# Kernel tuning notes

Hardware: AMD Instinct MI355X
Metric: run time of the kernel (lower is better)

The kernel has to match this reference:

```python
import jax, jax.numpy as jnp
import numpy as np

EMB = 768
HEADS = 12
DK = EMB // HEADS


def setup_inputs() -> dict:
    key = jax.random.key(0)
    ks = jax.random.split(key, 11)
    B, S = 2, 2048
    lim = 1.0 / np.sqrt(EMB)
    def lin(k):
        kw, kb = jax.random.split(k)
        W = jax.random.uniform(kw, (EMB, EMB), jnp.float32, -lim, lim)
        b = jax.random.uniform(kb, (EMB,), jnp.float32, -lim, lim)
        return W, b
    Wq, bq = lin(ks[0])
    Wk, bk = lin(ks[1])
    Wv, bv = lin(ks[2])
    Wo, bo = lin(ks[3])
    return {
        "query": jax.random.normal(ks[4], (B, S, EMB), jnp.float32),
        "key": jax.random.normal(ks[5], (B, S, EMB), jnp.float32),
        "value": jax.random.normal(ks[6], (B, S, EMB), jnp.float32),
        "Wq": Wq, "bq": bq, "Wk": Wk, "bk": bk,
        "Wv": Wv, "bv": bv, "Wo": Wo, "bo": bo,
    }


def reference(query, key, value, Wq, bq, Wk, bk, Wv, bv, Wo, bo):
    B, S, _ = query.shape
    # nn.Linear: x @ W^T + b, then split heads -> [B, H, S, d_k]
    def proj(x, W, b):
        return (x @ W.T + b).reshape(B, -1, HEADS, DK).transpose(0, 2, 1, 3)
    q = proj(query, Wq, bq)
    k = proj(key, Wk, bk)
    v = proj(value, Wv, bv)
    scale = 1.0 / jnp.sqrt(jnp.float32(DK))
    scores = jnp.einsum('bhqd,bhkd->bhqk', q, k) * scale  # [B,H,S,S]
    attn = jax.nn.softmax(scores, axis=-1)
    av = jnp.einsum('bhqk,bhkd->bhqd', attn, v)
    concat = av.transpose(0, 2, 1, 3).reshape(B, -1, EMB)
    return concat @ Wo.T + bo
```

## Files before the change

### kernel.cpp

```cpp
#include <hip/hip_runtime.h>
#include <hip/hip_bf16.h>

#define EMB 768
#define HEADS 12
#define DKV 64
#define BATCH 2
#define SEQ 2048
#define NTOK (BATCH*SEQ)

typedef float f32x4 __attribute__((ext_vector_type(4)));
typedef unsigned short u16;
typedef u16 u16x8 __attribute__((ext_vector_type(8)));
typedef u16 u16x4 __attribute__((ext_vector_type(4)));
typedef __bf16 bf16x8 __attribute__((ext_vector_type(8)));

__device__ __forceinline__ u16 f2bf(float f) {
  return __builtin_bit_cast(u16, (__bf16)f);
}
__device__ __forceinline__ float fexp2(float x) {
#if __has_builtin(__builtin_amdgcn_exp2f)
  return __builtin_amdgcn_exp2f(x);
#else
  return exp2f(x);
#endif
}
__device__ __forceinline__ f32x4 mfma16(u16x8 a, u16x8 b, f32x4 c) {
  return __builtin_amdgcn_mfma_f32_16x16x32_bf16(
      __builtin_bit_cast(bf16x8, a), __builtin_bit_cast(bf16x8, b), c, 0, 0, 0);
}
__device__ __forceinline__ void gload16(const void* g, void* l) {
  __builtin_amdgcn_global_load_lds(
      (const __attribute__((address_space(1))) void*)g,
      (__attribute__((address_space(3))) void*)l, 16, 0, 0);
}

__global__ void cast_all_k(
    const float* __restrict__ x0, const float* __restrict__ x1, const float* __restrict__ x2,
    const float* __restrict__ w0, const float* __restrict__ w1,
    const float* __restrict__ w2, const float* __restrict__ w3,
    u16* __restrict__ X0, u16* __restrict__ X1, u16* __restrict__ X2,
    u16* __restrict__ W0, u16* __restrict__ W1, u16* __restrict__ W2, u16* __restrict__ W3,
    float wscale0)
{
  const int NX = NTOK*EMB/8;
  const int NW = EMB*EMB/8;
  const int total = 3*NX + 4*NW;
  int i = blockIdx.x*256 + threadIdx.x;
  for (; i < total; i += gridDim.x*256) {
    const float* s; u16* d; int off; float sc = 1.f;
    if (i < 3*NX) {
      int which = i / NX; off = i - which*NX;
      s = which==0 ? x0 : which==1 ? x1 : x2;
      d = which==0 ? X0 : which==1 ? X1 : X2;
    } else {
      int j = i - 3*NX; int which = j / NW; off = j - which*NW;
      s = which==0 ? w0 : which==1 ? w1 : which==2 ? w2 : w3;
      d = which==0 ? W0 : which==1 ? W1 : which==2 ? W2 : W3;
      if (which == 0) sc = wscale0;
    }
    float4 a = reinterpret_cast<const float4*>(s)[off*2];
    float4 b = reinterpret_cast<const float4*>(s)[off*2+1];
    u16x8 o;
    o[0]=f2bf(a.x*sc); o[1]=f2bf(a.y*sc); o[2]=f2bf(a.z*sc); o[3]=f2bf(a.w*sc);
    o[4]=f2bf(b.x*sc); o[5]=f2bf(b.y*sc); o[6]=f2bf(b.z*sc); o[7]=f2bf(b.w*sc);
    reinterpret_cast<u16x8*>(d)[off] = o;
  }
}

template<int MODE>
__device__ __forceinline__ void gemm_core(
    const u16* __restrict__ A, const u16* __restrict__ Bm,
    const float* __restrict__ bias, float bscale, void* __restrict__ outp,
    u16* __restrict__ At, u16* __restrict__ Bt, int m0, int n0)
{
  const int t = threadIdx.x;
  const int w = t >> 6, lane = t & 63, lg = lane >> 4, lr = lane & 15;
  const int wr = w >> 1, wc = w & 1;

  f32x4 acc[2][4] = {};

  const int lrow = lane >> 3;
  const int csl  = lane & 7;

  auto STAGE = [&](int kb) {
    #pragma unroll
    for (int i = 0; i < 2; ++i) {
      int ci = w*2 + i;
      int row = ci*8 + lrow;
      int sg = csl ^ (row & 7);
      gload16(A + (size_t)(m0+row)*EMB + kb + sg*8, &At[ci*512]);
    }
    #pragma unroll
    for (int i = 0; i < 4; ++i) {
      int ci = w*4 + i;
      int row = ci*8 + lrow;
      int sg = csl ^ (row & 7);
      gload16(Bm + (size_t)(n0+row)*EMB + kb + sg*8, &Bt[ci*512]);
    }
  };

  auto COMPUTE = [&]() {
    u16x8 af[2][2], bf[4][2];
    #pragma unroll
    for (int fm = 0; fm < 2; ++fm)
      #pragma unroll
      for (int kk = 0; kk < 2; ++kk) {
        int r = wr*32 + fm*16 + lr;
        int p = (lg + 4*kk) ^ (r & 7);
        af[fm][kk] = *reinterpret_cast<const u16x8*>(&At[r*64 + p*8]);
      }
    #pragma unroll
    for (int fn = 0; fn < 4; ++fn)
      #pragma unroll
      for (int kk = 0; kk < 2; ++kk) {
        int r = wc*64 + fn*16 + lr;
        int p = (lg + 4*kk) ^ (r & 7);
        bf[fn][kk] = *reinterpret_cast<const u16x8*>(&Bt[r*64 + p*8]);
      }
    __builtin_amdgcn_s_setprio(1);
    #pragma unroll
    for (int fm = 0; fm < 2; ++fm)
      #pragma unroll
      for (int fn = 0; fn < 4; ++fn)
        #pragma unroll
        for (int kk = 0; kk < 2; ++kk)
          acc[fm][fn] = mfma16(af[fm][kk], bf[fn][kk], acc[fm][fn]);
    __builtin_amdgcn_s_setprio(0);
  };

  const int NSTEP = EMB/64;
  #pragma unroll
  for (int ts = 0; ts < NSTEP; ++ts) {
    STAGE(ts*64);
    __syncthreads();
    COMPUTE();
    if (ts+1 < NSTEP) __syncthreads();
  }

  #pragma unroll
  for (int fm = 0; fm < 2; ++fm)
    #pragma unroll
    for (int fn = 0; fn < 4; ++fn) {
      const int mb = m0 + wr*32 + fm*16 + lg*4;
      const int e  = n0 + wc*64 + fn*16 + lr;
      if constexpr (MODE == 2) {
        int bb = mb >> 11, sb = mb & 2047, h = e >> 6, d = e & 63;
        u16x4 o4;
        #pragma unroll
        for (int j = 0; j < 4; ++j) o4[j] = f2bf(acc[fm][fn][j] + bias[e]*bscale);
        *reinterpret_cast<u16x4*>(
            reinterpret_cast<u16*>(outp) + (((size_t)(bb*HEADS+h))*DKV + d)*SEQ + sb) = o4;
      } else {
        #pragma unroll
        for (int j = 0; j < 4; ++j) {
          int m = mb + j;
          float val = acc[fm][fn][j] + bias[e]*bscale;
          if constexpr (MODE == 0) {
            int bb = m >> 11, s = m & 2047, h = e >> 6, d = e & 63;
            reinterpret_cast<u16*>(outp)[(((size_t)(bb*HEADS+h))*SEQ + s)*DKV + d] = f2bf(val);
          } else {
            reinterpret_cast<float*>(outp)[(size_t)m*EMB + e] = val;
          }
        }
      }
    }
}

__global__ __launch_bounds__(256) void qkv_k(
    const u16* __restrict__ Xq, const u16* __restrict__ Xk, const u16* __restrict__ Xv,
    const u16* __restrict__ Wq, const u16* __restrict__ Wk, const u16* __restrict__ Wv,
    const float* __restrict__ bq, const float* __restrict__ bk, const float* __restrict__ bv,
    u16* __restrict__ Qh, u16* __restrict__ Kh, u16* __restrict__ Vh, float csc)
{
  __shared__ __align__(16) u16 At[64*64];
  __shared__ __align__(16) u16 Bt[128*64];
  const int m0 = blockIdx.x*64, n0 = blockIdx.y*128;
  const int z = blockIdx.z;
  if (z == 0)
    gemm_core<0>(Xq, Wq, bq, csc, Qh, At, Bt, m0, n0);
  else if (z == 1)
    gemm_core<0>(Xk, Wk, bk, 1.f, Kh, At, Bt, m0, n0);
  else
    gemm_core<2>(Xv, Wv, bv, 1.f, Vh, At, Bt, m0, n0);
}

__global__ __launch_bounds__(256) void gemm_out_k(
    const u16* __restrict__ A, const u16* __restrict__ Bm,
    const float* __restrict__ bias, float* __restrict__ outp)
{
  __shared__ __align__(16) u16 At[64*64];
  __shared__ __align__(16) u16 Bt[128*64];
  gemm_core<1>(A, Bm, bias, 1.f, outp, At, Bt, blockIdx.x*64, blockIdx.y*128);
}

__global__ __launch_bounds__(256) void flash_attn_k(
    const u16* __restrict__ Q, const u16* __restrict__ K, const u16* __restrict__ VT,
    u16* __restrict__ av)
{
  __shared__ __align__(16) u16 Kt[2][64*64];
  __shared__ __align__(16) u16 Vt[2][64*64];
  __shared__ __align__(16) u16 Pt[4][16*64];

  const int t = threadIdx.x;
  const int w = t >> 6, lane = t & 63, lg = lane >> 4, lr = lane & 15;
  const int tr = t >> 3, tsl = t & 7;
  const int qb = blockIdx.x;
  const int bh = blockIdx.y;
  const u16* Qb = Q  + (size_t)bh*SEQ*DKV;
  const u16* Kb = K  + (size_t)bh*SEQ*DKV;
  const u16* Vb = VT + (size_t)bh*DKV*SEQ;

  const int qrow = qb*64 + w*16 + lr;
  u16x8 qf[2];
  qf[0] = *reinterpret_cast<const u16x8*>(Qb + (size_t)qrow*DKV + lg*8);
  qf[1] = *reinterpret_cast<const u16x8*>(Qb + (size_t)qrow*DKV + 32 + lg*8);

  f32x4 acc[4] = {};
  float mrun = -1e30f, lrun = 0.f;

  u16x8 ks[2], vs[2];
  auto LOADKV = [&](int kt0) {
    #pragma unroll
    for (int q = 0; q < 2; ++q) {
      int row = q*32 + tr;
      ks[q] = *reinterpret_cast<const u16x8*>(Kb + (size_t)(kt0+row)*DKV + tsl*8);
    }
    #pragma unroll
    for (int q = 0; q < 2; ++q) {
      int d = q*32 + tr;
      vs[q] = *reinterpret_cast<const u16x8*>(Vb + (size_t)d*SEQ + kt0 + tsl*8);
    }
  };

  const int NT = SEQ/64;
  LOADKV(0);
  {
    #pragma unroll
    for (int q = 0; q < 2; ++q) {
      int row = q*32 + tr;
      *reinterpret_cast<u16x8*>(&Kt[0][row*64 + ((tsl ^ (row & 7))*8)]) = ks[q];
    }
    #pragma unroll
    for (int q = 0; q < 2; ++q) {
      int d = q*32 + tr;
      *reinterpret_cast<u16x8*>(&Vt[0][d*64 + ((tsl ^ (d & 7))*8)]) = vs[q];
    }
  }
  __syncthreads();

  char* Pw = reinterpret_cast<char*>(&Pt[w][0]);

#define TILE(bi, kt)                                                          \
  do {                                                                        \
    if ((kt)+1 < NT) LOADKV(((kt)+1)*64);                                     \
    f32x4 s[4];                                                               \
    __builtin_amdgcn_s_setprio(1);                                            \
    _Pragma("unroll")                                                         \
    for (int fc = 0; fc < 4; ++fc) {                                          \
      f32x4 z = {};                                                           \
      _Pragma("unroll")                                                       \
      for (int kk = 0; kk < 2; ++kk) {                                        \
        int r = fc*16 + lr;                                                   \
        int slot = (lg + 4*kk) ^ (r & 7);                                     \
        u16x8 kf = *reinterpret_cast<const u16x8*>(&Kt[bi][r*64 + slot*8]);   \
        z = mfma16(kf, qf[kk], z);                                            \
      }                                                                       \
      s[fc] = z;                                                              \
    }                                                                         \
    __builtin_amdgcn_s_setprio(0);                                            \
    float a0 = fmaxf(fmaxf(s[0][0], s[0][1]), s[0][2]);                       \
    float a1 = fmaxf(fmaxf(s[0][3], s[1][0]), s[1][1]);                       \
    float a2 = fmaxf(fmaxf(s[1][2], s[1][3]), s[2][0]);                       \
    float a3 = fmaxf(fmaxf(s[2][1], s[2][2]), s[2][3]);                       \
    float a4 = fmaxf(fmaxf(s[3][0], s[3][1]), s[3][2]);                       \
    float pmax = fmaxf(fmaxf(fmaxf(a0, a1), a2),                              \
                       fmaxf(fmaxf(a3, a4), s[3][3]));                        \
    if (__any(pmax > mrun + 8.f)) {          \
      float pm = fmaxf(pmax, __shfl_xor(pmax, 16));                           \
      pm = fmaxf(pm, __shfl_xor(pm, 32));                                     \
      float mnew = fmaxf(mrun, pm);                                           \
      float corr = fexp2(mrun - mnew);                                        \
      mrun = mnew; lrun *= corr;                                              \
      _Pragma("unroll")                                                       \
      for (int fc = 0; fc < 4; ++fc)                                          \
        _Pragma("unroll")                                                     \
        for (int j = 0; j < 4; ++j)                                           \
          acc[fc][j] *= corr;                                                 \
    }                                                                         \
    float p[4][4], rs[4];                                                     \
    _Pragma("unroll")                                                         \
    for (int fc = 0; fc < 4; ++fc) {                                          \
      _Pragma("unroll")                                                       \
      for (int j = 0; j < 4; ++j) p[fc][j] = fexp2(s[fc][j] - mrun);          \
      rs[fc] = (p[fc][0] + p[fc][1]) + (p[fc][2] + p[fc][3]);                 \
    }                                                                         \
    lrun += (rs[0] + rs[1]) + (rs[2] + rs[3]);      \
    _Pragma("unroll")                                                         \
    for (int fc = 0; fc < 4; ++fc) {                                          \
      u16x4 q4;                                                               \
      _Pragma("unroll")                                                       \
      for (int j = 0; j < 4; ++j) q4[j] = f2bf(p[fc][j]);                     \
      *reinterpret_cast<u16x4*>(                                              \
          Pw + lr*128 + (((fc*4 + lg) ^ ((lr & 7) << 1))*8)) = q4;            \
    }                                                                         \
    asm volatile("s_waitcnt lgkmcnt(0)" ::: "memory");                        \
    __builtin_amdgcn_sched_barrier(0);                                        \
    __builtin_amdgcn_s_setprio(1);                                            \
    _Pragma("unroll")                                                         \
    for (int kk = 0; kk < 2; ++kk) {                                          \
      u16x8 pf = *reinterpret_cast<const u16x8*>(                             \
          Pw + lr*128 + (((kk*8 + lg*2) ^ ((lr & 7) << 1))*8));               \
      _Pragma("unroll")                                                       \
      for (int fc = 0; fc < 4; ++fc) {                                        \
        int rv = fc*16 + lr;                                                  \
        int slotv = (lg + 4*kk) ^ (rv & 7);                                   \
        u16x8 vf = *reinterpret_cast<const u16x8*>(&Vt[bi][rv*64 + slotv*8]); \
        acc[fc] = mfma16(vf, pf, acc[fc]);                                    \
      }                                                                       \
    }                                                                         \
    __builtin_amdgcn_s_setprio(0);                                            \
    if ((kt)+1 < NT) {                                                        \
      _Pragma("unroll")                                                       \
      for (int q = 0; q < 2; ++q) {                                           \
        int row = q*32 + tr;                                                  \
        *reinterpret_cast<u16x8*>(                                            \
            &Kt[(bi)^1][row*64 + ((tsl ^ (row & 7))*8)]) = ks[q];             \
      }                                                                       \
      _Pragma("unroll")                                                       \
      for (int q = 0; q < 2; ++q) {                                           \
        int d = q*32 + tr;                                                    \
        *reinterpret_cast<u16x8*>(                                            \
            &Vt[(bi)^1][d*64 + ((tsl ^ (d & 7))*8)]) = vs[q];                 \
      }                                                                       \
    }                                                                         \
    __syncthreads();                                                          \
  } while (0)

  for (int kt = 0; kt < NT; kt += 2) {
    TILE(0, kt);
    TILE(1, kt+1);
  }
#undef TILE

  float lt = lrun;
  lt += __shfl_xor(lt, 16);
  lt += __shfl_xor(lt, 32);
  const float inv = 1.0f / lt;

  const int b = bh / HEADS, h = bh % HEADS;
  #pragma unroll
  for (int fc = 0; fc < 4; ++fc) {
    u16x4 o4;
    #pragma unroll
    for (int j = 0; j < 4; ++j) o4[j] = f2bf(acc[fc][j] * inv);
    *reinterpret_cast<u16x4*>(
        av + ((size_t)(b*SEQ + qrow))*EMB + h*64 + fc*16 + lg*4) = o4;
  }
}

extern "C" void kernel_launch(void* const* d_in, const int* in_sizes, int n_in,
                              void* d_out, int out_size, void* d_ws, size_t ws_size,
                              hipStream_t stream) {
  const float* xq_f = (const float*)d_in[0];
  const float* xk_f = (const float*)d_in[1];
  const float* xv_f = (const float*)d_in[2];
  const float* Wq = (const float*)d_in[3];
  const float* bq = (const float*)d_in[4];
  const float* Wk = (const float*)d_in[5];
  const float* bk = (const float*)d_in[6];
  const float* Wv = (const float*)d_in[7];
  const float* bv = (const float*)d_in[8];
  const float* Wo = (const float*)d_in[9];
  const float* bo = (const float*)d_in[10];

  const size_t NX = (size_t)NTOK*EMB;
  const size_t NW = (size_t)EMB*EMB;
  u16* Xc0 = (u16*)d_ws;
  u16* Xc1 = Xc0 + NX;
  u16* Xc2 = Xc1 + NX;
  u16* Wc0 = Xc2 + NX;
  u16* Wc1 = Wc0 + NW;
  u16* Wc2 = Wc1 + NW;
  u16* Wc3 = Wc2 + NW;
  u16* Qh  = Wc3 + NW;
  u16* Kh  = Qh + NX;
  u16* Vh  = Kh + NX;
  u16* Xb  = Xc0;

  const float csc = 0.125f * 1.4426950408889634f;

  cast_all_k<<<dim3(2048), dim3(256), 0, stream>>>(
      xq_f, xk_f, xv_f, Wq, Wk, Wv, Wo,
      Xc0, Xc1, Xc2, Wc0, Wc1, Wc2, Wc3, csc);

  qkv_k<<<dim3(NTOK/64, EMB/128, 3), dim3(256), 0, stream>>>(
      Xc0, Xc1, Xc2, Wc0, Wc1, Wc2, bq, bk, bv, Qh, Kh, Vh, csc);

  flash_attn_k<<<dim3(SEQ/64, BATCH*HEADS), dim3(256), 0, stream>>>(Qh, Kh, Vh, Xb);

  gemm_out_k<<<dim3(NTOK/64, EMB/128), dim3(256), 0, stream>>>(Xb, Wc3, bo, (float*)d_out);
}
```

Before: 96.39 us.

## Fuse activation fp32-to-bf16 cast into QKV GEMM and use async LDS loads in attention

```diff
diff --git a/kernel.cpp b/kernel.cpp
--- a/kernel.cpp
+++ b/kernel.cpp
@@ -34,62 +34,72 @@
       (__attribute__((address_space(3))) void*)l, 16, 0, 0);
 }
 
-__global__ void cast_all_k(
-    const float* __restrict__ x0, const float* __restrict__ x1, const float* __restrict__ x2,
+__global__ void cast_w_k(
     const float* __restrict__ w0, const float* __restrict__ w1,
     const float* __restrict__ w2, const float* __restrict__ w3,
-    u16* __restrict__ X0, u16* __restrict__ X1, u16* __restrict__ X2,
-    u16* __restrict__ W0, u16* __restrict__ W1, u16* __restrict__ W2, u16* __restrict__ W3,
-    float wscale0)
+    u16* __restrict__ W0, u16* __restrict__ W1, u16* __restrict__ W2, u16* __restrict__ W3)
 {
-  const int NX = NTOK*EMB/8;
   const int NW = EMB*EMB/8;
-  const int total = 3*NX + 4*NW;
   int i = blockIdx.x*256 + threadIdx.x;
-  for (; i < total; i += gridDim.x*256) {
-    const float* s; u16* d; int off; float sc = 1.f;
-    if (i < 3*NX) {
-      int which = i / NX; off = i - which*NX;
-      s = which==0 ? x0 : which==1 ? x1 : x2;
-      d = which==0 ? X0 : which==1 ? X1 : X2;
-    } else {
-      int j = i - 3*NX; int which = j / NW; off = j - which*NW;
-      s = which==0 ? w0 : which==1 ? w1 : which==2 ? w2 : w3;
-      d = which==0 ? W0 : which==1 ? W1 : which==2 ? W2 : W3;
-      if (which == 0) sc = wscale0;
-    }
-    float4 a = reinterpret_cast<const float4*>(s)[off*2];
-    float4 b = reinterpret_cast<const float4*>(s)[off*2+1];
-    u16x8 o;
-    o[0]=f2bf(a.x*sc); o[1]=f2bf(a.y*sc); o[2]=f2bf(a.z*sc); o[3]=f2bf(a.w*sc);
-    o[4]=f2bf(b.x*sc); o[5]=f2bf(b.y*sc); o[6]=f2bf(b.z*sc); o[7]=f2bf(b.w*sc);
-    reinterpret_cast<u16x8*>(d)[off] = o;
-  }
-}
-
-template<int MODE>
+  if (i >= 4*NW) return;
+  int which = i / NW, off = i - which*NW;
+  const float* s = which==0 ? w0 : which==1 ? w1 : which==2 ? w2 : w3;
+  u16* d        = which==0 ? W0 : which==1 ? W1 : which==2 ? W2 : W3;
+  float4 a = reinterpret_cast<const float4*>(s)[off*2];
+  float4 b = reinterpret_cast<const float4*>(s)[off*2+1];
+  u16x8 o;
+  o[0]=f2bf(a.x); o[1]=f2bf(a.y); o[2]=f2bf(a.z); o[3]=f2bf(a.w);
+  o[4]=f2bf(b.x); o[5]=f2bf(b.y); o[6]=f2bf(b.z); o[7]=f2bf(b.w);
+  reinterpret_cast<u16x8*>(d)[off] = o;
+}
+
+template<int MODE, bool AF32>
 __device__ __forceinline__ void gemm_core(
-    const u16* __restrict__ A, const u16* __restrict__ Bm,
-    const float* __restrict__ bias, float bscale, void* __restrict__ outp,
-    u16* __restrict__ At, u16* __restrict__ Bt, int m0, int n0)
+    const void* __restrict__ Ap, const u16* __restrict__ Bm,
+    const float* __restrict__ bias, float ascale, float bscale,
+    void* __restrict__ outp, u16* __restrict__ At, u16* __restrict__ Bt,
+    int m0, int n0)
 {
   const int t = threadIdx.x;
   const int w = t >> 6, lane = t & 63, lg = lane >> 4, lr = lane & 15;
   const int wr = w >> 1, wc = w & 1;
+  const int lrow = lane >> 3, csl = lane & 7;
 
   f32x4 acc[2][4] = {};
-
-  const int lrow = lane >> 3;
-  const int csl  = lane & 7;
-
-  auto STAGE = [&](int kb) {
+  f32x4 raf[2][2];
+
+  auto A_LOAD = [&](int kb) {
+    #pragma unroll
+    for (int q2 = 0; q2 < 2; ++q2) {
+      int c = q2*256 + t, row = c >> 3, sl = c & 7;
+      const float* p = (const float*)Ap + (size_t)(m0+row)*EMB + kb + sl*8;
+      raf[q2][0] = *reinterpret_cast<const f32x4*>(p);
+      raf[q2][1] = *reinterpret_cast<const f32x4*>(p + 4);
+    }
+  };
+  auto A_WRITE = [&]() {
+    #pragma unroll
+    for (int q2 = 0; q2 < 2; ++q2) {
+      int c = q2*256 + t, row = c >> 3, sl = c & 7;
+      u16x8 v;
+      #pragma unroll
+      for (int j = 0; j < 4; ++j) {
+        v[j]   = f2bf(raf[q2][0][j] * ascale);
+        v[4+j] = f2bf(raf[q2][1][j] * ascale);
+      }
+      *reinterpret_cast<u16x8*>(&At[row*64 + ((sl ^ (row & 7))*8)]) = v;
+    }
+  };
+  auto A_GLOAD = [&](int kb) {
     #pragma unroll
     for (int i = 0; i < 2; ++i) {
       int ci = w*2 + i;
       int row = ci*8 + lrow;
       int sg = csl ^ (row & 7);
-      gload16(A + (size_t)(m0+row)*EMB + kb + sg*8, &At[ci*512]);
-    }
+      gload16((const u16*)Ap + (size_t)(m0+row)*EMB + kb + sg*8, &At[ci*512]);
+    }
+  };
+  auto B_GLOAD = [&](int kb) {
     #pragma unroll
     for (int i = 0; i < 4; ++i) {
       int ci = w*4 + i;
@@ -129,12 +139,31 @@
   };
 
   const int NSTEP = EMB/64;
-  #pragma unroll
-  for (int ts = 0; ts < NSTEP; ++ts) {
-    STAGE(ts*64);
+  if constexpr (AF32) {
+    A_LOAD(0);
+    B_GLOAD(0);
+    A_WRITE();
     __syncthreads();
-    COMPUTE();
-    if (ts+1 < NSTEP) __syncthreads();
+    #pragma unroll
+    for (int ts = 0; ts < NSTEP; ++ts) {
+      if (ts+1 < NSTEP) A_LOAD((ts+1)*64);
+      COMPUTE();
+      if (ts+1 < NSTEP) {
+        __syncthreads();
+        B_GLOAD((ts+1)*64);
+        A_WRITE();
+        __syncthreads();
+      }
+    }
+  } else {
+    #pragma unroll
+    for (int ts = 0; ts < NSTEP; ++ts) {
+      A_GLOAD(ts*64);
+      B_GLOAD(ts*64);
+      __syncthreads();
+      COMPUTE();
+      if (ts+1 < NSTEP) __syncthreads();
+    }
   }
 
   #pragma unroll
@@ -167,7 +196,7 @@
 }
 
 __global__ __launch_bounds__(256) void qkv_k(
-    const u16* __restrict__ Xq, const u16* __restrict__ Xk, const u16* __restrict__ Xv,
+    const float* __restrict__ Xq, const float* __restrict__ Xk, const float* __restrict__ Xv,
     const u16* __restrict__ Wq, const u16* __restrict__ Wk, const u16* __restrict__ Wv,
     const float* __restrict__ bq, const float* __restrict__ bk, const float* __restrict__ bv,
     u16* __restrict__ Qh, u16* __restrict__ Kh, u16* __restrict__ Vh, float csc)
@@ -177,11 +206,11 @@
   const int m0 = blockIdx.x*64, n0 = blockIdx.y*128;
   const int z = blockIdx.z;
   if (z == 0)
-    gemm_core<0>(Xq, Wq, bq, csc, Qh, At, Bt, m0, n0);
+    gemm_core<0,true>(Xq, Wq, bq, csc, csc, Qh, At, Bt, m0, n0);
   else if (z == 1)
-    gemm_core<0>(Xk, Wk, bk, 1.f, Kh, At, Bt, m0, n0);
+    gemm_core<0,true>(Xk, Wk, bk, 1.f, 1.f, Kh, At, Bt, m0, n0);
   else
-    gemm_core<2>(Xv, Wv, bv, 1.f, Vh, At, Bt, m0, n0);
+    gemm_core<2,true>(Xv, Wv, bv, 1.f, 1.f, Vh, At, Bt, m0, n0);
 }
 
 __global__ __launch_bounds__(256) void gemm_out_k(
@@ -190,7 +219,7 @@
 {
   __shared__ __align__(16) u16 At[64*64];
   __shared__ __align__(16) u16 Bt[128*64];
-  gemm_core<1>(A, Bm, bias, 1.f, outp, At, Bt, blockIdx.x*64, blockIdx.y*128);
+  gemm_core<1,false>(A, Bm, bias, 1.f, 1.f, outp, At, Bt, blockIdx.x*64, blockIdx.y*128);
 }
 
 __global__ __launch_bounds__(256) void flash_attn_k(
@@ -203,7 +232,6 @@
 
   const int t = threadIdx.x;
   const int w = t >> 6, lane = t & 63, lg = lane >> 4, lr = lane & 15;
-  const int tr = t >> 3, tsl = t & 7;
   const int qb = blockIdx.x;
   const int bh = blockIdx.y;
   const u16* Qb = Q  + (size_t)bh*SEQ*DKV;
@@ -218,41 +246,29 @@
   f32x4 acc[4] = {};
   float mrun = -1e30f, lrun = 0.f;
 
-  u16x8 ks[2], vs[2];
-  auto LOADKV = [&](int kt0) {
-    #pragma unroll
-    for (int q = 0; q < 2; ++q) {
-      int row = q*32 + tr;
-      ks[q] = *reinterpret_cast<const u16x8*>(Kb + (size_t)(kt0+row)*DKV + tsl*8);
-    }
-    #pragma unroll
-    for (int q = 0; q < 2; ++q) {
-      int d = q*32 + tr;
-      vs[q] = *reinterpret_cast<const u16x8*>(Vb + (size_t)d*SEQ + kt0 + tsl*8);
+  auto STAGE = [&](int kt0, int bi) {
+    #pragma unroll
+    for (int c2 = 0; c2 < 2; ++c2) {
+      int c = c2*256 + t;
+      int row = c >> 3, sl = c & 7;
+      int sg = sl ^ (row & 7);
+      gload16(Kb + (size_t)(kt0+row)*DKV + sg*8, &Kt[bi][c*8]);
+    }
+    #pragma unroll
+    for (int c2 = 0; c2 < 2; ++c2) {
+      int c = c2*256 + t;
+      int row = c >> 3, sl = c & 7;
+      int sg = sl ^ (row & 7);
+      gload16(Vb + (size_t)row*SEQ + kt0 + sg*8, &Vt[bi][c*8]);
     }
   };
 
   const int NT = SEQ/64;
-  LOADKV(0);
-  {
-    #pragma unroll
-    for (int q = 0; q < 2; ++q) {
-      int row = q*32 + tr;
-      *reinterpret_cast<u16x8*>(&Kt[0][row*64 + ((tsl ^ (row & 7))*8)]) = ks[q];
-    }
-    #pragma unroll
-    for (int q = 0; q < 2; ++q) {
-      int d = q*32 + tr;
-      *reinterpret_cast<u16x8*>(&Vt[0][d*64 + ((tsl ^ (d & 7))*8)]) = vs[q];
-    }
-  }
-  __syncthreads();
-
   char* Pw = reinterpret_cast<char*>(&Pt[w][0]);
 
 #define TILE(bi, kt)                                                          \
   do {                                                                        \
-    if ((kt)+1 < NT) LOADKV(((kt)+1)*64);                                     \
+    if ((kt)+1 < NT) STAGE(((kt)+1)*64, (bi)^1);    \
     f32x4 s[4];                                                               \
     __builtin_amdgcn_s_setprio(1);                                            \
     _Pragma("unroll")                                                         \
@@ -319,23 +335,11 @@
       }                                                                       \
     }                                                                         \
     __builtin_amdgcn_s_setprio(0);                                            \
-    if ((kt)+1 < NT) {                                                        \
-      _Pragma("unroll")                                                       \
-      for (int q = 0; q < 2; ++q) {                                           \
-        int row = q*32 + tr;                                                  \
-        *reinterpret_cast<u16x8*>(                                            \
-            &Kt[(bi)^1][row*64 + ((tsl ^ (row & 7))*8)]) = ks[q];             \
-      }                                                                       \
-      _Pragma("unroll")                                                       \
-      for (int q = 0; q < 2; ++q) {                                           \
-        int d = q*32 + tr;                                                    \
-        *reinterpret_cast<u16x8*>(                                            \
-            &Vt[(bi)^1][d*64 + ((tsl ^ (d & 7))*8)]) = vs[q];                 \
-      }                                                                       \
-    }                                                                         \
-    __syncthreads();                                                          \
+    __syncthreads();   \
   } while (0)
 
+  STAGE(0, 0);
+  __syncthreads();
   for (int kt = 0; kt < NT; kt += 2) {
     TILE(0, kt);
     TILE(1, kt+1);
@@ -375,26 +379,22 @@
 
   const size_t NX = (size_t)NTOK*EMB;
   const size_t NW = (size_t)EMB*EMB;
-  u16* Xc0 = (u16*)d_ws;
-  u16* Xc1 = Xc0 + NX;
-  u16* Xc2 = Xc1 + NX;
-  u16* Wc0 = Xc2 + NX;
+  u16* Wc0 = (u16*)d_ws;
   u16* Wc1 = Wc0 + NW;
   u16* Wc2 = Wc1 + NW;
   u16* Wc3 = Wc2 + NW;
   u16* Qh  = Wc3 + NW;
   u16* Kh  = Qh + NX;
   u16* Vh  = Kh + NX;
-  u16* Xb  = Xc0;
+  u16* Xb  = Vh + NX;
 
   const float csc = 0.125f * 1.4426950408889634f;
 
-  cast_all_k<<<dim3(2048), dim3(256), 0, stream>>>(
-      xq_f, xk_f, xv_f, Wq, Wk, Wv, Wo,
-      Xc0, Xc1, Xc2, Wc0, Wc1, Wc2, Wc3, csc);
+  cast_w_k<<<dim3(4*EMB*EMB/8/256), dim3(256), 0, stream>>>(
+      Wq, Wk, Wv, Wo, Wc0, Wc1, Wc2, Wc3);
 
   qkv_k<<<dim3(NTOK/64, EMB/128, 3), dim3(256), 0, stream>>>(
-      Xc0, Xc1, Xc2, Wc0, Wc1, Wc2, bq, bk, bv, Qh, Kh, Vh, csc);
+      xq_f, xk_f, xv_f, Wc0, Wc1, Wc2, bq, bk, bv, Qh, Kh, Vh, csc);
 
   flash_attn_k<<<dim3(SEQ/64, BATCH*HEADS), dim3(256), 0, stream>>>(Qh, Kh, Vh, Xb);
 
```

New measurement: 96.01 us. No clear change (-0.4%).
